# Optimization experiments

Measured on AMD Instinct MI355X. Metric: run time of the kernel, lower is better.

## Reference

```python
import jax, jax.numpy as jnp
import numpy as np

CLASS_NUM = 512
B = 32768

def setup_inputs() -> dict:
    key = jax.random.key(0)
    k1, k2 = jax.random.split(key)
    output = jax.random.normal(k1, (B, CLASS_NUM), dtype=jnp.float32)
    target = jax.random.randint(k2, (B, CLASS_NUM), 0, 2, dtype=jnp.int32)
    return {"output": output, "target": target}

def reference(output, target):
    # pos/neg masks; labels are guaranteed 0/1
    pos = (target == 1).astype(output.dtype)  # [B, C]
    neg = (target == 0).astype(output.dtype)  # [B, C]
    # sum_{p in pos, q in neg} exp(o_q - o_p) = (sum_q neg*e^{o_q}) * (sum_p pos*e^{-o_p})
    s_neg = jnp.sum(neg * jnp.exp(output), axis=-1)   # [B]
    s_pos = jnp.sum(pos * jnp.exp(-output), axis=-1)  # [B]
    num = jnp.sum(pos, axis=-1) * jnp.sum(neg, axis=-1)  # |pos|*|neg|
    num = jnp.where(num == 0, jnp.asarray(CLASS_NUM, output.dtype), num)
    loss = jnp.sum(s_neg * s_pos / num)
    return loss
```

## Files before the change

kernel.cpp:

```cpp
#include <hip/hip_runtime.h>

#define CLS 512
#define NROWS 32768
#define WPB 4
#define NBLOCKS 2048
#define TOTAL_WAVES (NBLOCKS * WPB)

__global__ __launch_bounds__(256) void lr_partial_kernel(
    const float* __restrict__ out, const int* __restrict__ tgt,
    float* __restrict__ partial) {
  const int lane = threadIdx.x & 63;
  const int wid  = threadIdx.x >> 6;
  const int gw   = blockIdx.x * WPB + wid;

  float acc = 0.0f;

  for (int row = gw; row < NROWS; row += TOTAL_WAVES) {
    const float4* po = reinterpret_cast<const float4*>(out + (size_t)row * CLS) + lane * 2;
    const int4*   pt = reinterpret_cast<const int4*>(tgt + (size_t)row * CLS) + lane * 2;
    float4 o0 = po[0];
    float4 o1 = po[1];
    int4   t0 = pt[0];
    int4   t1 = pt[1];

    float ov[8] = {o0.x, o0.y, o0.z, o0.w, o1.x, o1.y, o1.z, o1.w};
    int   tv[8] = {t0.x, t0.y, t0.z, t0.w, t1.x, t1.y, t1.z, t1.w};

    float s_neg = 0.0f, s_pos = 0.0f;
    int npos = 0;
#pragma unroll
    for (int j = 0; j < 8; ++j) {
      float x = tv[j] ? -ov[j] : ov[j];
      float e = __expf(x);
      if (tv[j]) { s_pos += e; npos += 1; }
      else       { s_neg += e; }
    }

#pragma unroll
    for (int m = 1; m < 64; m <<= 1) {
      s_neg += __shfl_xor(s_neg, m);
      s_pos += __shfl_xor(s_pos, m);
      npos  += __shfl_xor(npos, m);
    }

    float fpos = (float)npos;
    float fneg = (float)(CLS - npos);
    float num  = fpos * fneg;
    if (num == 0.0f) num = (float)CLS;
    acc += s_neg * s_pos / num;
  }

  __shared__ float sacc[WPB];
  if (lane == 0) sacc[wid] = acc;
  __syncthreads();
  if (threadIdx.x == 0) {
    float s = 0.0f;
#pragma unroll
    for (int i = 0; i < WPB; ++i) s += sacc[i];
    partial[blockIdx.x] = s;
  }
}

__global__ __launch_bounds__(256) void lr_final_kernel(
    const float* __restrict__ partial, float* __restrict__ out) {
  const int lane = threadIdx.x & 63;
  const int wid  = threadIdx.x >> 6;

  float s = 0.0f;
  for (int i = threadIdx.x; i < NBLOCKS; i += 256) s += partial[i];

#pragma unroll
  for (int m = 1; m < 64; m <<= 1) s += __shfl_xor(s, m);

  __shared__ float w[4];
  if (lane == 0) w[wid] = s;
  __syncthreads();
  if (threadIdx.x == 0) out[0] = w[0] + w[1] + w[2] + w[3];
}

extern "C" void kernel_launch(void* const* d_in, const int* in_sizes, int n_in,
                              void* d_out, int out_size, void* d_ws, size_t ws_size,
                              hipStream_t stream) {
  const float* output = (const float*)d_in[0];
  const int*   target = (const int*)d_in[1];
  float* partial = (float*)d_ws;
  float* loss    = (float*)d_out;

  lr_partial_kernel<<<NBLOCKS, 256, 0, stream>>>(output, target, partial);
  lr_final_kernel<<<1, 256, 0, stream>>>(partial, loss);
}
```

Before: 28.35 us.

## Process four rows per wave with 16-lane groups and atomic final reduction

Each wave now handles four rows at once, with 16 lanes per row each loading 8 float4/int4 pairs, so more loads are in flight per thread and the shuffle reduction tree is shorter. The per-element branch becomes a select, and the positive count is accumulated in float. The second reduction kernel is replaced by a memset plus one atomicAdd per block. This trades a kernel launch for 2048 float atomics on one address and a summation order that is no longer deterministic.

```diff
diff --git a/kernel.cpp b/kernel.cpp
--- a/kernel.cpp
+++ b/kernel.cpp
@@ -4,78 +4,56 @@
 #define NROWS 32768
 #define WPB 4
 #define NBLOCKS 2048
-#define TOTAL_WAVES (NBLOCKS * WPB)
 
-__global__ __launch_bounds__(256) void lr_partial_kernel(
+__global__ __launch_bounds__(256) void lr_kernel(
     const float* __restrict__ out, const int* __restrict__ tgt,
-    float* __restrict__ partial) {
+    float* __restrict__ loss) {
   const int lane = threadIdx.x & 63;
-  const int wid  = threadIdx.x >> 6;
-  const int gw   = blockIdx.x * WPB + wid;
+  const int s    = lane & 15;
+  const int gw   = blockIdx.x * WPB + (threadIdx.x >> 6);
+  const int row  = gw * 4 + (lane >> 4);
 
-  float acc = 0.0f;
+  const float* op = out + (size_t)row * CLS + s * 4;
+  const int*   tp = tgt + (size_t)row * CLS + s * 4;
 
-  for (int row = gw; row < NROWS; row += TOTAL_WAVES) {
-    const float4* po = reinterpret_cast<const float4*>(out + (size_t)row * CLS) + lane * 2;
-    const int4*   pt = reinterpret_cast<const int4*>(tgt + (size_t)row * CLS) + lane * 2;
-    float4 o0 = po[0];
-    float4 o1 = po[1];
-    int4   t0 = pt[0];
-    int4   t1 = pt[1];
-
-    float ov[8] = {o0.x, o0.y, o0.z, o0.w, o1.x, o1.y, o1.z, o1.w};
-    int   tv[8] = {t0.x, t0.y, t0.z, t0.w, t1.x, t1.y, t1.z, t1.w};
-
-    float s_neg = 0.0f, s_pos = 0.0f;
-    int npos = 0;
+  float s_neg = 0.0f, s_pos = 0.0f, np = 0.0f;
 #pragma unroll
-    for (int j = 0; j < 8; ++j) {
-      float x = tv[j] ? -ov[j] : ov[j];
-      float e = __expf(x);
-      if (tv[j]) { s_pos += e; npos += 1; }
-      else       { s_neg += e; }
+  for (int p = 0; p < 8; ++p) {
+    float4 o = *reinterpret_cast<const float4*>(op + p * 64);
+    int4   t = *reinterpret_cast<const int4*>(tp + p * 64);
+    float ov[4] = {o.x, o.y, o.z, o.w};
+    int   tv[4] = {t.x, t.y, t.z, t.w};
+#pragma unroll
+    for (int j = 0; j < 4; ++j) {
+      float e = __expf(tv[j] ? -ov[j] : ov[j]);
+      s_pos += tv[j] ? e : 0.0f;
+      s_neg += tv[j] ? 0.0f : e;
+      np    += tv[j] ? 1.0f : 0.0f;
     }
+  }
 
 #pragma unroll
-    for (int m = 1; m < 64; m <<= 1) {
-      s_neg += __shfl_xor(s_neg, m);
-      s_pos += __shfl_xor(s_pos, m);
-      npos  += __shfl_xor(npos, m);
-    }
-
-    float fpos = (float)npos;
-    float fneg = (float)(CLS - npos);
-    float num  = fpos * fneg;
-    if (num == 0.0f) num = (float)CLS;
-    acc += s_neg * s_pos / num;
+  for (int m = 1; m < 16; m <<= 1) {
+    s_neg += __shfl_xor(s_neg, m);
+    s_pos += __shfl_xor(s_pos, m);
+    np    += __shfl_xor(np, m);
   }
 
+  float fneg = (float)CLS - np;
+  float num  = np * fneg;
+  if (num == 0.0f) num = (float)CLS;
+  float c = (s == 0) ? s_neg * s_pos / num : 0.0f;
+
+  c += __shfl_xor(c, 16);
+  c += __shfl_xor(c, 32);
+
   __shared__ float sacc[WPB];
-  if (lane == 0) sacc[wid] = acc;
+  if (lane == 0) sacc[threadIdx.x >> 6] = c;
   __syncthreads();
   if (threadIdx.x == 0) {
-    float s = 0.0f;
-#pragma unroll
-    for (int i = 0; i < WPB; ++i) s += sacc[i];
-    partial[blockIdx.x] = s;
+    float t = sacc[0] + sacc[1] + sacc[2] + sacc[3];
+    atomicAdd(loss, t);
   }
-}
-
-__global__ __launch_bounds__(256) void lr_final_kernel(
-    const float* __restrict__ partial, float* __restrict__ out) {
-  const int lane = threadIdx.x & 63;
-  const int wid  = threadIdx.x >> 6;
-
-  float s = 0.0f;
-  for (int i = threadIdx.x; i < NBLOCKS; i += 256) s += partial[i];
-
-#pragma unroll
-  for (int m = 1; m < 64; m <<= 1) s += __shfl_xor(s, m);
-
-  __shared__ float w[4];
-  if (lane == 0) w[wid] = s;
-  __syncthreads();
-  if (threadIdx.x == 0) out[0] = w[0] + w[1] + w[2] + w[3];
 }
 
 extern "C" void kernel_launch(void* const* d_in, const int* in_sizes, int n_in,
@@ -83,9 +61,8 @@
                               hipStream_t stream) {
   const float* output = (const float*)d_in[0];
   const int*   target = (const int*)d_in[1];
-  float* partial = (float*)d_ws;
-  float* loss    = (float*)d_out;
+  float* loss = (float*)d_out;
 
-  lr_partial_kernel<<<NBLOCKS, 256, 0, stream>>>(output, target, partial);
-  lr_final_kernel<<<1, 256, 0, stream>>>(partial, loss);
+  hipMemsetAsync(loss, 0, sizeof(float), stream);
+  lr_kernel<<<NBLOCKS, 256, 0, stream>>>(output, target, loss);
 }
```

Result: slower. 44.88 us (+58.3%).

## Assign contiguous four-row chunks per wave and issue all loads upfront

Applied to the files above, without the earlier changes.

Each wave now owns four consecutive rows and issues all sixteen 16-byte loads before any computation, replacing the grid-stride loop. Lanes read consecutive float4s instead of pairs, so each load instruction is fully contiguous across the wave. The per-element branches become selects and the positive count is kept as a float. The aim is more memory-level parallelism and better coalescing, at the cost of more registers per thread and a hardcoded assumption that NBLOCKS*WPB*4 equals NROWS.

```diff
diff --git a/kernel.cpp b/kernel.cpp
--- a/kernel.cpp
+++ b/kernel.cpp
@@ -4,48 +4,53 @@
 #define NROWS 32768
 #define WPB 4
 #define NBLOCKS 2048
-#define TOTAL_WAVES (NBLOCKS * WPB)
 
-__global__ __launch_bounds__(256) void lr_partial_kernel(
+__global__ __launch_bounds__(256) void lr_main_kernel(
     const float* __restrict__ out, const int* __restrict__ tgt,
     float* __restrict__ partial) {
   const int lane = threadIdx.x & 63;
   const int wid  = threadIdx.x >> 6;
   const int gw   = blockIdx.x * WPB + wid;
+  const size_t base = (size_t)gw * 4 * CLS;
+
+  const float4* po = reinterpret_cast<const float4*>(out + base);
+  const int4*   pt = reinterpret_cast<const int4*>(tgt + base);
+
+  float4 o[8];
+  int4   t[8];
+#pragma unroll
+  for (int r = 0; r < 4; ++r) {
+    o[2 * r]     = po[r * 128 + lane];
+    o[2 * r + 1] = po[r * 128 + 64 + lane];
+    t[2 * r]     = pt[r * 128 + lane];
+    t[2 * r + 1] = pt[r * 128 + 64 + lane];
+  }
 
   float acc = 0.0f;
-
-  for (int row = gw; row < NROWS; row += TOTAL_WAVES) {
-    const float4* po = reinterpret_cast<const float4*>(out + (size_t)row * CLS) + lane * 2;
-    const int4*   pt = reinterpret_cast<const int4*>(tgt + (size_t)row * CLS) + lane * 2;
-    float4 o0 = po[0];
-    float4 o1 = po[1];
-    int4   t0 = pt[0];
-    int4   t1 = pt[1];
-
-    float ov[8] = {o0.x, o0.y, o0.z, o0.w, o1.x, o1.y, o1.z, o1.w};
-    int   tv[8] = {t0.x, t0.y, t0.z, t0.w, t1.x, t1.y, t1.z, t1.w};
-
-    float s_neg = 0.0f, s_pos = 0.0f;
-    int npos = 0;
 #pragma unroll
-    for (int j = 0; j < 8; ++j) {
-      float x = tv[j] ? -ov[j] : ov[j];
-      float e = __expf(x);
-      if (tv[j]) { s_pos += e; npos += 1; }
-      else       { s_neg += e; }
+  for (int r = 0; r < 4; ++r) {
+    float s_neg = 0.0f, s_pos = 0.0f, np = 0.0f;
+#pragma unroll
+    for (int k = 0; k < 2; ++k) {
+      float4 ov = o[2 * r + k];
+      int4   tv = t[2 * r + k];
+      float vx[4] = {ov.x, ov.y, ov.z, ov.w};
+      int   mx[4] = {tv.x, tv.y, tv.z, tv.w};
+#pragma unroll
+      for (int j = 0; j < 4; ++j) {
+        float e = __expf(mx[j] ? -vx[j] : vx[j]);
+        s_pos += mx[j] ? e : 0.0f;
+        s_neg += mx[j] ? 0.0f : e;
+        np    += mx[j] ? 1.0f : 0.0f;
+      }
     }
-
 #pragma unroll
     for (int m = 1; m < 64; m <<= 1) {
       s_neg += __shfl_xor(s_neg, m);
       s_pos += __shfl_xor(s_pos, m);
-      npos  += __shfl_xor(npos, m);
+      np    += __shfl_xor(np, m);
     }
-
-    float fpos = (float)npos;
-    float fneg = (float)(CLS - npos);
-    float num  = fpos * fneg;
+    float num = np * ((float)CLS - np);
     if (num == 0.0f) num = (float)CLS;
     acc += s_neg * s_pos / num;
   }
@@ -53,12 +58,8 @@
   __shared__ float sacc[WPB];
   if (lane == 0) sacc[wid] = acc;
   __syncthreads();
-  if (threadIdx.x == 0) {
-    float s = 0.0f;
-#pragma unroll
-    for (int i = 0; i < WPB; ++i) s += sacc[i];
-    partial[blockIdx.x] = s;
-  }
+  if (threadIdx.x == 0)
+    partial[blockIdx.x] = sacc[0] + sacc[1] + sacc[2] + sacc[3];
 }
 
 __global__ __launch_bounds__(256) void lr_final_kernel(
@@ -67,6 +68,7 @@
   const int wid  = threadIdx.x >> 6;
 
   float s = 0.0f;
+#pragma unroll
   for (int i = threadIdx.x; i < NBLOCKS; i += 256) s += partial[i];
 
 #pragma unroll
@@ -86,6 +88,6 @@
   float* partial = (float*)d_ws;
   float* loss    = (float*)d_out;
 
-  lr_partial_kernel<<<NBLOCKS, 256, 0, stream>>>(output, target, partial);
+  lr_main_kernel<<<NBLOCKS, 256, 0, stream>>>(output, target, partial);
   lr_final_kernel<<<1, 256, 0, stream>>>(partial, loss);
 }
```

Result: faster. 27.59 us (-2.7%).
